# Performance work log

Hardware: AMD Instinct MI355X
Metric: run time of the kernel (lower is better)

## Reference

```python
import jax, jax.numpy as jnp
import numpy as np

N_NODES = 50000
N_EDGES = 800000
D = 64
NUM_GRAPHS = 64


def setup_inputs() -> dict:
    key = jax.random.key(0)
    ks = jax.random.split(key, 8)
    node_features = jax.random.normal(ks[0], (N_NODES, D), dtype=jnp.float32)
    edge_index = jax.random.randint(ks[1], (2, N_EDGES), 0, N_NODES, dtype=jnp.int32)
    edge_weight = jax.random.uniform(ks[2], (N_EDGES,), dtype=jnp.float32)
    batch = jnp.sort(jax.random.randint(ks[3], (N_NODES,), 0, NUM_GRAPHS, dtype=jnp.int32))
    scale = 1.0 / np.sqrt(D)
    W1 = jax.random.normal(ks[4], (D, D), dtype=jnp.float32) * scale
    b1 = jnp.zeros((D,), dtype=jnp.float32)
    W2 = jax.random.normal(ks[5], (D, D), dtype=jnp.float32) * scale
    b2 = jnp.zeros((D,), dtype=jnp.float32)
    return {"node_features": node_features, "edge_index": edge_index,
            "edge_weight": edge_weight, "batch": batch,
            "W1": W1, "b1": b1, "W2": W2, "b2": b2}


def gcn_conv(x, row, col, ew, W, b, n_nodes):
    # PyG GCNConv: add self-loops (weight 1), symmetric normalization,
    # x' = norm-weighted scatter of (x @ W) over edges, plus bias.
    loop = jnp.arange(n_nodes, dtype=row.dtype)
    r = jnp.concatenate([row, loop])
    c = jnp.concatenate([col, loop])
    w = jnp.concatenate([ew, jnp.ones((n_nodes,), dtype=ew.dtype)])
    deg = jax.ops.segment_sum(w, c, num_segments=n_nodes)  # [N]
    dis = jnp.where(deg > 0, jax.lax.rsqrt(deg), 0.0)
    norm = dis[r] * w * dis[c]                             # [E+N]
    xw = x @ W                                             # [N, D_out]
    msg = xw[r] * norm[:, None]                            # gather + scale
    out = jax.ops.segment_sum(msg, c, num_segments=n_nodes)
    return out + b


def reference(node_features, edge_index, edge_weight, batch, W1, b1, W2, b2):
    row, col = edge_index[0], edge_index[1]
    x = node_features.astype(jnp.float32)
    # conv layers (all but final pooling layer) each followed by ReLU
    x = jax.nn.relu(gcn_conv(x, row, col, edge_weight, W1, b1, N_NODES))
    x = jax.nn.relu(gcn_conv(x, row, col, edge_weight, W2, b2, N_NODES))
    # MeanAggregation pooling over graph ids
    sums = jax.ops.segment_sum(x, batch, num_segments=NUM_GRAPHS)       # [G, D]
    cnts = jax.ops.segment_sum(jnp.ones((x.shape[0],), x.dtype), batch,
                               num_segments=NUM_GRAPHS)                 # [G]
    return sums / jnp.maximum(cnts, 1.0)[:, None]
```

## Files before the change

### kernel.cpp

```cpp
#include <hip/hip_runtime.h>
#include <hip/hip_fp16.h>

#define NN 50000
#define NE 800000
#define DD 64
#define NG 64

#define NBKT 196
#define MAXB 5120
#define SRTB 7168
#define P1CH 4096
#define P1NB ((NE + P1CH - 1) / P1CH)

__global__ __launch_bounds__(256) void bin_k(const int* __restrict__ ei,
                                             const float* __restrict__ ew,
                                             int* __restrict__ bucket_cnt,
                                             unsigned int* __restrict__ tmp_pay,
                                             unsigned char* __restrict__ tmp_c8) {
    __shared__ int hist[NBKT];
    __shared__ int basec[NBKT];
    const int t = threadIdx.x;
    const int e0 = blockIdx.x * P1CH;
    for (int i = t; i < NBKT; i += 256) hist[i] = 0;
    __syncthreads();
    int rr[16]; int cc[16]; float wwf[16];
    #pragma unroll
    for (int i = 0; i < 16; ++i) {
        int e = e0 + i * 256 + t;
        if (e < NE) {
            rr[i] = ei[e]; cc[i] = ei[NE + e]; wwf[i] = ew[e];
            atomicAdd(&hist[cc[i] >> 8], 1);
        } else cc[i] = -1;
    }
    __syncthreads();
    for (int i = t; i < NBKT; i += 256)
        basec[i] = (hist[i] > 0) ? (i * MAXB + atomicAdd(&bucket_cnt[i], hist[i])) : 0;
    __syncthreads();
    #pragma unroll
    for (int i = 0; i < 16; ++i) {
        if (cc[i] >= 0) {
            int b = cc[i] >> 8;
            int slot = atomicAdd(&basec[b], 1);
            unsigned int hb = (unsigned int)__half_as_ushort(__float2half(wwf[i]));
            tmp_pay[slot] = (hb << 16) | (unsigned int)rr[i];
            tmp_c8[slot] = (unsigned char)(cc[i] & 255);
        }
    }
}

__global__ __launch_bounds__(256) void build_k(const int* __restrict__ bucket_cnt,
                                               const unsigned int* __restrict__ tmp_pay,
                                               const unsigned char* __restrict__ tmp_c8,
                                               unsigned int* __restrict__ srt,
                                               int2* __restrict__ rowse,
                                               float* __restrict__ dis) {
    __shared__ int hist[256];
    __shared__ int cursor[256];
    __shared__ float degf[256];
    __shared__ int wtot[4];
    const int b = blockIdx.x;
    const int t = threadIdx.x;
    const int cntb = bucket_cnt[b];
    const int tbase = b * MAXB;
    hist[t] = 0; degf[t] = 0.0f;
    __syncthreads();
    for (int i = t; i < cntb; i += 256) atomicAdd(&hist[tmp_c8[tbase + i]], 1);
    __syncthreads();
    const int v = hist[t];
    const int pv = (v + 7) & ~7;
    int pre = pv;
    #pragma unroll
    for (int off = 1; off < 64; off <<= 1) {
        int u = __shfl_up(pre, off);
        if ((t & 63) >= off) pre += u;
    }
    if ((t & 63) == 63) wtot[t >> 6] = pre;
    __syncthreads();
    int woff = 0;
    for (int i = 0; i < (t >> 6); ++i) woff += wtot[i];
    const int start = b * SRTB + woff + pre - pv;
    cursor[t] = start;
    __syncthreads();
    for (int i = t; i < cntb; i += 256) {
        unsigned int u = tmp_pay[tbase + i];
        int c8 = tmp_c8[tbase + i];
        int slot = atomicAdd(&cursor[c8], 1);
        srt[slot] = u;
        float w = __half2float(__ushort_as_half((unsigned short)(u >> 16)));
        atomicAdd(&degf[c8], w);
    }
    __syncthreads();
    for (int i = start + v; i < start + pv; ++i) srt[i] = 0u;
    const int node = b * 256 + t;
    if (node < NN) {
        rowse[node] = make_int2(start, pv);
        dis[node] = rsqrtf(1.0f + degf[t]);
    }
}

template<bool ACT>
__global__ __launch_bounds__(256, 4) void gemm_k(
    const float* __restrict__ X, const float* __restrict__ W,
    const float* __restrict__ bias_prev, const float* __restrict__ dis,
    __half* __restrict__ Ah)
{
    __shared__ float Ws[64][64];
    __shared__ float Xs[64][68];
    const int t = threadIdx.x;
    const int row0 = blockIdx.x * 64;

    #pragma unroll
    for (int s = t; s < 64 * 64; s += 256) ((float*)Ws)[s] = W[s];
    #pragma unroll
    for (int s = t; s < 64 * 64; s += 256) {
        int r = s >> 6, k = s & 63;
        int row = row0 + r;
        if (row >= NN) row = NN - 1;
        float v = X[(size_t)row * DD + k];
        if (ACT) v = fmaxf(v + bias_prev[k], 0.0f);
        Xs[r][k] = v;
    }
    __syncthreads();

    const int tc = t & 15;
    const int tr = t >> 4;
    float4 acc[4];
    #pragma unroll
    for (int i = 0; i < 4; ++i) acc[i] = make_float4(0.f, 0.f, 0.f, 0.f);

    #pragma unroll 2
    for (int kc = 0; kc < 16; ++kc) {
        const int k = kc * 4;
        float4 w0 = *reinterpret_cast<const float4*>(&Ws[k + 0][tc * 4]);
        float4 w1 = *reinterpret_cast<const float4*>(&Ws[k + 1][tc * 4]);
        float4 w2 = *reinterpret_cast<const float4*>(&Ws[k + 2][tc * 4]);
        float4 w3 = *reinterpret_cast<const float4*>(&Ws[k + 3][tc * 4]);
        #pragma unroll
        for (int i = 0; i < 4; ++i) {
            float4 xv = *reinterpret_cast<const float4*>(&Xs[tr * 4 + i][k]);
            acc[i].x += xv.x * w0.x + xv.y * w1.x + xv.z * w2.x + xv.w * w3.x;
            acc[i].y += xv.x * w0.y + xv.y * w1.y + xv.z * w2.y + xv.w * w3.y;
            acc[i].z += xv.x * w0.z + xv.y * w1.z + xv.z * w2.z + xv.w * w3.z;
            acc[i].w += xv.x * w0.w + xv.y * w1.w + xv.z * w2.w + xv.w * w3.w;
        }
    }

    #pragma unroll
    for (int i = 0; i < 4; ++i) {
        int row = row0 + tr * 4 + i;
        if (row >= NN) break;
        float d = dis[row];
        __half2 h0 = __floats2half2_rn(acc[i].x * d, acc[i].y * d);
        __half2 h1 = __floats2half2_rn(acc[i].z * d, acc[i].w * d);
        uint2 st;
        st.x = *reinterpret_cast<unsigned int*>(&h0);
        st.y = *reinterpret_cast<unsigned int*>(&h1);
        *reinterpret_cast<uint2*>(&Ah[(size_t)row * DD + tc * 4]) = st;
    }
}

__global__ __launch_bounds__(256) void gather_k(
    const int2* __restrict__ rowse, const unsigned int* __restrict__ srt,
    const float* __restrict__ dis,
    const __half* __restrict__ Ah, float* __restrict__ B)
{
    const int node = blockIdx.x * 4 + (threadIdx.x >> 6);
    const int lane = threadIdx.x & 63;
    if (node >= NN) return;
    const int2 se = rowse[node];
    float acc0 = __half2float(Ah[(size_t)node * DD + lane]);
    float acc1 = 0.0f, acc2 = 0.0f, acc3 = 0.0f;
    const unsigned int* p = srt + se.x;
    uint4 u0 = *reinterpret_cast<const uint4*>(p);
    uint4 u1 = *reinterpret_cast<const uint4*>(p + 4);
    for (int n = se.y; n > 0; n -= 8) {
        uint4 n0, n1;
        if (n > 8) {
            p += 8;
            n0 = *reinterpret_cast<const uint4*>(p);
            n1 = *reinterpret_cast<const uint4*>(p + 4);
        }
        __half h0 = Ah[(size_t)(u0.x & 0xffffu) * DD + lane];
        __half h1 = Ah[(size_t)(u0.y & 0xffffu) * DD + lane];
        __half h2 = Ah[(size_t)(u0.z & 0xffffu) * DD + lane];
        __half h3 = Ah[(size_t)(u0.w & 0xffffu) * DD + lane];
        __half h4 = Ah[(size_t)(u1.x & 0xffffu) * DD + lane];
        __half h5 = Ah[(size_t)(u1.y & 0xffffu) * DD + lane];
        __half h6 = Ah[(size_t)(u1.z & 0xffffu) * DD + lane];
        __half h7 = Ah[(size_t)(u1.w & 0xffffu) * DD + lane];
        acc0 += __half2float(__ushort_as_half((unsigned short)(u0.x >> 16))) * __half2float(h0);
        acc1 += __half2float(__ushort_as_half((unsigned short)(u0.y >> 16))) * __half2float(h1);
        acc2 += __half2float(__ushort_as_half((unsigned short)(u0.z >> 16))) * __half2float(h2);
        acc3 += __half2float(__ushort_as_half((unsigned short)(u0.w >> 16))) * __half2float(h3);
        acc0 += __half2float(__ushort_as_half((unsigned short)(u1.x >> 16))) * __half2float(h4);
        acc1 += __half2float(__ushort_as_half((unsigned short)(u1.y >> 16))) * __half2float(h5);
        acc2 += __half2float(__ushort_as_half((unsigned short)(u1.z >> 16))) * __half2float(h6);
        acc3 += __half2float(__ushort_as_half((unsigned short)(u1.w >> 16))) * __half2float(h7);
        u0 = n0; u1 = n1;
    }
    B[(size_t)node * DD + lane] = dis[node] * ((acc0 + acc1) + (acc2 + acc3));
}

__global__ __launch_bounds__(64) void pool(
    const float* __restrict__ B, const float* __restrict__ b2,
    const int* __restrict__ batch,
    float* __restrict__ sums, float* __restrict__ cnts, int n)
{
    const int lane = threadIdx.x;
    const int start = blockIdx.x * 32;
    const int end = min(start + 32, n);
    const float bb = b2[lane];
    float acc = 0.0f;
    int cn = 0;
    int curg = batch[start];
    for (int i = start; i < end; ++i) {
        int g = batch[i];
        if (g != curg) {
            unsafeAtomicAdd(&sums[curg * DD + lane], acc);
            if (lane == 0) unsafeAtomicAdd(&cnts[curg], (float)cn);
            acc = 0.0f; cn = 0; curg = g;
        }
        acc += fmaxf(B[(size_t)i * DD + lane] + bb, 0.0f);
        cn++;
    }
    if (cn > 0) {
        unsafeAtomicAdd(&sums[curg * DD + lane], acc);
        if (lane == 0) unsafeAtomicAdd(&cnts[curg], (float)cn);
    }
}

__global__ void finalize(const float* __restrict__ sums, const float* __restrict__ cnts,
                         float* __restrict__ out) {
    int i = blockIdx.x * blockDim.x + threadIdx.x;
    if (i < NG * DD) {
        int g = i >> 6;
        out[i] = sums[i] / fmaxf(cnts[g], 1.0f);
    }
}

extern "C" void kernel_launch(void* const* d_in, const int* in_sizes, int n_in,
                              void* d_out, int out_size, void* d_ws, size_t ws_size,
                              hipStream_t stream) {
    const float* x   = (const float*)d_in[0];
    const int*   ei  = (const int*)  d_in[1];
    const float* ew  = (const float*)d_in[2];
    const int*   bat = (const int*)  d_in[3];
    const float* W1  = (const float*)d_in[4];
    const float* b1  = (const float*)d_in[5];
    const float* W2  = (const float*)d_in[6];
    const float* b2  = (const float*)d_in[7];
    float* out = (float*)d_out;

    char* ws = (char*)d_ws;
    size_t off = 0;
    __half* Ah        = (__half*)(ws + off); off += (size_t)NN * DD * 2;
    float*  B         = (float*) (ws + off); off += (size_t)NN * DD * 4;
    unsigned int* srt = (unsigned int*)(ws + off); off += (size_t)NBKT * SRTB * 4;
    unsigned int* tmp_pay = (unsigned int*)(ws + off); off += (size_t)NBKT * MAXB * 4;
    unsigned char* tmp_c8 = (unsigned char*)(ws + off); off += (size_t)NBKT * MAXB;
    int2*   rowse      = (int2*)(ws + off); off += (size_t)NN * 8;
    float*  dis        = (float*)(ws + off); off += (size_t)NN * 4;
    int*    bucket_cnt = (int*)  (ws + off); off += (size_t)NBKT * 4;
    float*  sums       = (float*)(ws + off); off += (size_t)NG * DD * 4;
    float*  cnts       = (float*)(ws + off); off += (size_t)NG * 4;

    (void)hipMemsetAsync(bucket_cnt, 0, (size_t)(NBKT + NG * DD + NG) * 4, stream);

    bin_k<<<P1NB, 256, 0, stream>>>(ei, ew, bucket_cnt, tmp_pay, tmp_c8);
    build_k<<<NBKT, 256, 0, stream>>>(bucket_cnt, tmp_pay, tmp_c8, srt, rowse, dis);

    gemm_k<false><<<(NN + 63) / 64, 256, 0, stream>>>(x, W1, nullptr, dis, Ah);
    gather_k<<<(NN + 3) / 4, 256, 0, stream>>>(rowse, srt, dis, Ah, B);

    gemm_k<true><<<(NN + 63) / 64, 256, 0, stream>>>(B, W2, b1, dis, Ah);
    gather_k<<<(NN + 3) / 4, 256, 0, stream>>>(rowse, srt, dis, Ah, B);

    pool<<<(NN + 31) / 32, 64, 0, stream>>>(B, b2, bat, sums, cnts, NN);
    finalize<<<(NG * DD + 255) / 256, 256, 0, stream>>>(sums, cnts, out);
}
```

Before: 142.3 us.

## Fuse layer-1 gather with layer-2 GEMM and halve binning chunk size

Adds a fused kernel that performs the layer-1 neighbor gather (with normalization, bias and ReLU) into shared memory and immediately multiplies it by W2, writing the scaled half-precision result for the second gather. This removes the fp32 intermediate B round-trip and one kernel launch between the first gather and second GEMM. The bin kernel also processes 2048 edges per block instead of 4096, doubling block count for more parallelism but more global atomics on bucket counters. The fused kernel has fewer concurrent gathering waves per node block, which may reduce latency hiding for the irregular gathers.

After: 151.7 us. 1.07x slower.

```diff
diff --git a/kernel.cpp b/kernel.cpp
--- a/kernel.cpp
+++ b/kernel.cpp
@@ -9,7 +9,7 @@
 #define NBKT 196
 #define MAXB 5120
 #define SRTB 7168
-#define P1CH 4096
+#define P1CH 2048
 #define P1NB ((NE + P1CH - 1) / P1CH)
 
 __global__ __launch_bounds__(256) void bin_k(const int* __restrict__ ei,
@@ -23,9 +23,9 @@
     const int e0 = blockIdx.x * P1CH;
     for (int i = t; i < NBKT; i += 256) hist[i] = 0;
     __syncthreads();
-    int rr[16]; int cc[16]; float wwf[16];
-    #pragma unroll
-    for (int i = 0; i < 16; ++i) {
+    int rr[8]; int cc[8]; float wwf[8];
+    #pragma unroll
+    for (int i = 0; i < 8; ++i) {
         int e = e0 + i * 256 + t;
         if (e < NE) {
             rr[i] = ei[e]; cc[i] = ei[NE + e]; wwf[i] = ew[e];
@@ -37,7 +37,7 @@
         basec[i] = (hist[i] > 0) ? (i * MAXB + atomicAdd(&bucket_cnt[i], hist[i])) : 0;
     __syncthreads();
     #pragma unroll
-    for (int i = 0; i < 16; ++i) {
+    for (int i = 0; i < 8; ++i) {
         if (cc[i] >= 0) {
             int b = cc[i] >> 8;
             int slot = atomicAdd(&basec[b], 1);
@@ -156,6 +156,102 @@
         st.x = *reinterpret_cast<unsigned int*>(&h0);
         st.y = *reinterpret_cast<unsigned int*>(&h1);
         *reinterpret_cast<uint2*>(&Ah[(size_t)row * DD + tc * 4]) = st;
+    }
+}
+
+__global__ __launch_bounds__(256, 4) void fused_k(
+    const int2* __restrict__ rowse, const unsigned int* __restrict__ srt,
+    const float* __restrict__ dis, const __half* __restrict__ Ah,
+    const float* __restrict__ W, const float* __restrict__ bias_prev,
+    __half* __restrict__ Aout)
+{
+    __shared__ float Ws[64][64];
+    __shared__ float Xs[64][68];
+    const int t = threadIdx.x;
+    const int w = t >> 6, lane = t & 63;
+    const int row0 = blockIdx.x * 64;
+
+    #pragma unroll
+    for (int s = t; s < 64 * 64; s += 256) ((float*)Ws)[s] = W[s];
+
+    const float bb = bias_prev[lane];
+
+    for (int i = 0; i < 16; ++i) {
+        const int rl = w * 16 + i;
+        const int node = row0 + rl;
+        float res = 0.0f;
+        if (node < NN) {
+            const int2 se = rowse[node];
+            float acc0 = __half2float(Ah[(size_t)node * DD + lane]);
+            float acc1 = 0.0f, acc2 = 0.0f, acc3 = 0.0f;
+            const unsigned int* p = srt + se.x;
+            uint4 u0 = *reinterpret_cast<const uint4*>(p);
+            uint4 u1 = *reinterpret_cast<const uint4*>(p + 4);
+            for (int n = se.y; n > 0; n -= 8) {
+                uint4 n0, n1;
+                if (n > 8) {
+                    p += 8;
+                    n0 = *reinterpret_cast<const uint4*>(p);
+                    n1 = *reinterpret_cast<const uint4*>(p + 4);
+                }
+                __half h0 = Ah[(size_t)(u0.x & 0xffffu) * DD + lane];
+                __half h1 = Ah[(size_t)(u0.y & 0xffffu) * DD + lane];
+                __half h2 = Ah[(size_t)(u0.z & 0xffffu) * DD + lane];
+                __half h3 = Ah[(size_t)(u0.w & 0xffffu) * DD + lane];
+                __half h4 = Ah[(size_t)(u1.x & 0xffffu) * DD + lane];
+                __half h5 = Ah[(size_t)(u1.y & 0xffffu) * DD + lane];
+                __half h6 = Ah[(size_t)(u1.z & 0xffffu) * DD + lane];
+                __half h7 = Ah[(size_t)(u1.w & 0xffffu) * DD + lane];
+                acc0 += __half2float(__ushort_as_half((unsigned short)(u0.x >> 16))) * __half2float(h0);
+                acc1 += __half2float(__ushort_as_half((unsigned short)(u0.y >> 16))) * __half2float(h1);
+                acc2 += __half2float(__ushort_as_half((unsigned short)(u0.z >> 16))) * __half2float(h2);
+                acc3 += __half2float(__ushort_as_half((unsigned short)(u0.w >> 16))) * __half2float(h3);
+                acc0 += __half2float(__ushort_as_half((unsigned short)(u1.x >> 16))) * __half2float(h4);
+                acc1 += __half2float(__ushort_as_half((unsigned short)(u1.y >> 16))) * __half2float(h5);
+                acc2 += __half2float(__ushort_as_half((unsigned short)(u1.z >> 16))) * __half2float(h6);
+                acc3 += __half2float(__ushort_as_half((unsigned short)(u1.w >> 16))) * __half2float(h7);
+                u0 = n0; u1 = n1;
+            }
+            res = fmaxf(dis[node] * ((acc0 + acc1) + (acc2 + acc3)) + bb, 0.0f);
+        }
+        Xs[rl][lane] = res;
+    }
+    __syncthreads();
+
+    const int tc = t & 15;
+    const int tr = t >> 4;
+    float4 acc[4];
+    #pragma unroll
+    for (int i = 0; i < 4; ++i) acc[i] = make_float4(0.f, 0.f, 0.f, 0.f);
+
+    #pragma unroll 2
+    for (int kc = 0; kc < 16; ++kc) {
+        const int k = kc * 4;
+        float4 w0 = *reinterpret_cast<const float4*>(&Ws[k + 0][tc * 4]);
+        float4 w1 = *reinterpret_cast<const float4*>(&Ws[k + 1][tc * 4]);
+        float4 w2 = *reinterpret_cast<const float4*>(&Ws[k + 2][tc * 4]);
+        float4 w3 = *reinterpret_cast<const float4*>(&Ws[k + 3][tc * 4]);
+        #pragma unroll
+        for (int i = 0; i < 4; ++i) {
+            float4 xv = *reinterpret_cast<const float4*>(&Xs[tr * 4 + i][k]);
+            acc[i].x += xv.x * w0.x + xv.y * w1.x + xv.z * w2.x + xv.w * w3.x;
+            acc[i].y += xv.x * w0.y + xv.y * w1.y + xv.z * w2.y + xv.w * w3.y;
+            acc[i].z += xv.x * w0.z + xv.y * w1.z + xv.z * w2.z + xv.w * w3.z;
+            acc[i].w += xv.x * w0.w + xv.y * w1.w + xv.z * w2.w + xv.w * w3.w;
+        }
+    }
+
+    #pragma unroll
+    for (int i = 0; i < 4; ++i) {
+        int row = row0 + tr * 4 + i;
+        if (row >= NN) break;
+        float d = dis[row];
+        __half2 h0 = __floats2half2_rn(acc[i].x * d, acc[i].y * d);
+        __half2 h1 = __floats2half2_rn(acc[i].z * d, acc[i].w * d);
+        uint2 st;
+        st.x = *reinterpret_cast<unsigned int*>(&h0);
+        st.y = *reinterpret_cast<unsigned int*>(&h1);
+        *reinterpret_cast<uint2*>(&Aout[(size_t)row * DD + tc * 4]) = st;
     }
 }
 
@@ -254,6 +350,7 @@
     char* ws = (char*)d_ws;
     size_t off = 0;
     __half* Ah        = (__half*)(ws + off); off += (size_t)NN * DD * 2;
+    __half* Ah2       = (__half*)(ws + off); off += (size_t)NN * DD * 2;
     float*  B         = (float*) (ws + off); off += (size_t)NN * DD * 4;
     unsigned int* srt = (unsigned int*)(ws + off); off += (size_t)NBKT * SRTB * 4;
     unsigned int* tmp_pay = (unsigned int*)(ws + off); off += (size_t)NBKT * MAXB * 4;
@@ -270,10 +367,8 @@
     build_k<<<NBKT, 256, 0, stream>>>(bucket_cnt, tmp_pay, tmp_c8, srt, rowse, dis);
 
     gemm_k<false><<<(NN + 63) / 64, 256, 0, stream>>>(x, W1, nullptr, dis, Ah);
-    gather_k<<<(NN + 3) / 4, 256, 0, stream>>>(rowse, srt, dis, Ah, B);
-
-    gemm_k<true><<<(NN + 63) / 64, 256, 0, stream>>>(B, W2, b1, dis, Ah);
-    gather_k<<<(NN + 3) / 4, 256, 0, stream>>>(rowse, srt, dis, Ah, B);
+    fused_k<<<(NN + 63) / 64, 256, 0, stream>>>(rowse, srt, dis, Ah, W2, b1, Ah2);
+    gather_k<<<(NN + 3) / 4, 256, 0, stream>>>(rowse, srt, dis, Ah2, B);
 
     pool<<<(NN + 31) / 32, 64, 0, stream>>>(B, b2, bat, sums, cnts, NN);
     finalize<<<(NG * DD + 255) / 256, 256, 0, stream>>>(sums, cnts, out);
```
